# Performance work log

Measured on AMD Instinct MI355X. Metric: run time of the kernel, lower is better.

## Reference

```python
import jax, jax.numpy as jnp
import numpy as np

B, T_TEXT, HID = 16, 512, 512
MAX_LEN = 2048
DP_CH, DP_K = 256, 3
PP_CH, PP_K, PP_LAYERS = 384, 5, 5
N_BINS = 256


def conv1d_same(x, w, b, pad):
    # x: [B, C_in, T], w: [C_out, C_in, K] -> [B, C_out, T]
    xp = jnp.pad(x, ((0, 0), (0, 0), (pad, pad)))
    y = jax.lax.conv_general_dilated(xp, w, (1,), 'VALID',
                                     dimension_numbers=('NCH', 'OIH', 'NCH'))
    return y + b[None, :, None]


def channel_ln(x, g, beta, eps=1e-5):
    # LayerNorm over channel dim of [B, C, T] (torch LayerNorm with dim=1)
    m = jnp.mean(x, axis=1, keepdims=True)
    v = jnp.mean((x - m) ** 2, axis=1, keepdims=True)
    return (x - m) / jnp.sqrt(v + eps) * g[None, :, None] + beta[None, :, None]


def sinusoidal_pos(T, dim):
    # fairseq-style sinusoidal embedding, positions start at padding_idx+1 = 1
    half = dim // 2
    inv = jnp.exp(jnp.arange(half, dtype=jnp.float32) * (-np.log(10000.0) / (half - 1)))
    pos = jnp.arange(1, T + 1, dtype=jnp.float32)
    ang = pos[:, None] * inv[None, :]
    return jnp.concatenate([jnp.sin(ang), jnp.cos(ang)], axis=1)  # [T, dim]


def setup_inputs() -> dict:
    key = jax.random.key(0)
    ks = jax.random.split(key, 16)
    sd = lambda fan: 1.0 / np.sqrt(fan)
    inp = {}
    inp['x'] = jax.random.normal(ks[0], (B, T_TEXT, HID), dtype=jnp.float32)
    inp['duration'] = jax.random.randint(ks[1], (B, T_TEXT), 0, 7, dtype=jnp.int32)
    inp['src_mask'] = jnp.zeros((B, T_TEXT), dtype=bool)
    inp['max_len'] = MAX_LEN
    # duration predictor params (2 conv layers + linear)
    inp['dp_w0'] = jax.random.normal(ks[2], (DP_CH, HID, DP_K)) * sd(HID * DP_K)
    inp['dp_w1'] = jax.random.normal(ks[3], (DP_CH, DP_CH, DP_K)) * sd(DP_CH * DP_K)
    inp['dp_b'] = jnp.zeros((2, DP_CH))
    inp['dp_g'] = jnp.ones((2, DP_CH))
    inp['dp_beta'] = jnp.zeros((2, DP_CH))
    inp['dp_lin_w'] = jax.random.normal(ks[4], (DP_CH, 1)) * sd(DP_CH)
    inp['dp_lin_b'] = jnp.zeros((1,))
    # pitch predictor params (5 conv layers + linear, odim=2 for use_uv)
    inp['pp_w0'] = jax.random.normal(ks[5], (PP_CH, HID, PP_K)) * sd(HID * PP_K)
    inp['pp_w_rest'] = jax.random.normal(ks[6], (PP_LAYERS - 1, PP_CH, PP_CH, PP_K)) * sd(PP_CH * PP_K)
    inp['pp_b'] = jnp.zeros((PP_LAYERS, PP_CH))
    inp['pp_g'] = jnp.ones((PP_LAYERS, PP_CH))
    inp['pp_beta'] = jnp.zeros((PP_LAYERS, PP_CH))
    inp['pp_lin_w'] = jax.random.normal(ks[7], (PP_CH, 2)) * sd(PP_CH)
    inp['pp_lin_b'] = jnp.zeros((2,))
    inp['pos_alpha'] = jnp.ones((1,))
    inp['pitch_emb'] = jax.random.normal(ks[8], (N_BINS, HID)) * 0.02
    inp['pitch_bins'] = jnp.linspace(-1.0, 1.0, N_BINS - 1)  # linear quantization, stats min/max
    return inp


def reference(x, duration, src_mask, max_len, dp_w0, dp_w1, dp_b, dp_g, dp_beta,
              dp_lin_w, dp_lin_b, pp_w0, pp_w_rest, pp_b, pp_g, pp_beta,
              pp_lin_w, pp_lin_b, pos_alpha, pitch_emb, pitch_bins):
    Bn, T, H = x.shape
    keep = 1.0 - src_mask.astype(x.dtype)  # [B,T], 1 where valid

    # ---- DurationPredictor (log-domain durations) ----
    h = jnp.transpose(x, (0, 2, 1))  # [B,H,T]
    for i, w in enumerate([dp_w0, dp_w1]):
        h = conv1d_same(h, w, dp_b[i], (DP_K - 1) // 2)
        h = jax.nn.relu(h)
        h = channel_ln(h, dp_g[i], dp_beta[i])
        h = h * keep[:, None, :]
    log_dur = (jnp.einsum('bct,co->bto', h, dp_lin_w) + dp_lin_b) * keep[:, :, None]
    log_dur = log_dur[..., 0]  # [B,T]

    # ---- LengthRegulator: vectorized variable-repeat via searchsorted ----
    cum = jnp.cumsum(duration, axis=1)  # [B,T]
    frames = jnp.arange(max_len)
    tok = jax.vmap(lambda c: jnp.searchsorted(c, frames, side='right'))(cum)  # [B,max_len]
    mel_len = cum[:, -1]
    fmask = (frames[None, :] < mel_len[:, None]).astype(x.dtype)  # [B,max_len]
    mel = jnp.take_along_axis(x, jnp.minimum(tok, T - 1)[..., None], axis=1) * fmask[..., None]

    # ---- VariancePredictor (pitch, odim=2 for f0 + uv) ----
    pe = sinusoidal_pos(max_len, H)  # [max_len, H]
    p = mel + pos_alpha[0] * pe[None]
    p = jnp.transpose(p, (0, 2, 1))  # [B,H,max_len]
    for i in range(PP_LAYERS):
        w = pp_w0 if i == 0 else pp_w_rest[i - 1]
        p = conv1d_same(p, w, pp_b[i], (PP_K - 1) // 2)
        p = jax.nn.relu(p)
        p = channel_ln(p, pp_g[i], pp_beta[i])
    pitch_pred = jnp.einsum('bct,co->bto', p, pp_lin_w) + pp_lin_b  # [B,max_len,2]

    # ---- bucketize f0 channel + embedding add ----
    idx = jnp.searchsorted(pitch_bins, pitch_pred[..., 0], side='left')  # torch.bucketize
    p_embed = pitch_emb[idx]  # [B,max_len,H]
    out = mel + p_embed
    return out, log_dur, pitch_pred, mel_len
```

## Files before the change

kernel.cpp:

```cpp
#include <hip/hip_runtime.h>
#include <cstdint>
#include <cstddef>

constexpr int BB      = 16;
constexpr int T_TEXT  = 512;
constexpr int HID     = 512;
constexpr int MAX_LEN = 2048;
constexpr int DP_CH   = 256;
constexpr int PP_CH   = 384;

typedef unsigned short u16;
typedef unsigned int   u32;
typedef short bf16x8 __attribute__((ext_vector_type(8)));
typedef float f32x4  __attribute__((ext_vector_type(4)));

__device__ __forceinline__ void gload_lds16(const void* g, void* l) {
  __builtin_amdgcn_global_load_lds(
      (const __attribute__((address_space(1))) u32*)g,
      (__attribute__((address_space(3))) u32*)l, 16, 0, 0);
}

__device__ __forceinline__ u16 f2bf(float v) {
  union { float f; u32 u; } a;
  a.f = v;
  u32 r = (a.u + 0x7FFFu + ((a.u >> 16) & 1u)) >> 16;
  return (u16)r;
}
__device__ __forceinline__ float bf2f(u16 h) {
  union { u32 u; float f; } a;
  a.u = (u32)h << 16;
  return a.f;
}

__global__ __launch_bounds__(256) void pack_w_k(const float* __restrict__ w,
                                                u16* __restrict__ p,
                                                int O, int I, int KT) {
  int NF  = O >> 4, NCB = I >> 5;
  int total = KT * NCB * NF * 64;
  int idx = blockIdx.x * 256 + threadIdx.x;
  if (idx >= total) return;
  int l  = idx & 63;
  int f  = (idx >> 6) % NF;
  int cb = ((idx >> 6) / NF) % NCB;
  int k  = (idx >> 6) / (NF * NCB);
  int o  = f * 16 + (l & 15);
  int ib = cb * 32 + (l >> 4) * 8;
  u16* pd = p + ((size_t)((k * NCB + cb) * NF + f)) * 512 + (size_t)l * 8;
#pragma unroll
  for (int j = 0; j < 8; ++j)
    pd[j] = f2bf(w[((size_t)o * I + ib + j) * KT + k]);
}

template <int CIN, int COUT, int KT, int MT, int WM, int WN, int OPAD,
          bool F32OUT, bool ROTATE>
__global__ __launch_bounds__(WM * WN * 64)
void gemm_conv_ln(const u16* __restrict__ a, const u16* __restrict__ wp,
                  const float* __restrict__ bias, const float* __restrict__ gamma,
                  const float* __restrict__ beta,
                  u16* __restrict__ o, float* __restrict__ fo, int T) {
  constexpr int WAVES   = WM * WN;
  constexpr int THREADS = WAVES * 64;
  constexpr int RS    = MT + KT - 1;
  constexpr int NCB   = CIN / 32;
  constexpr int NF    = COUT / 16;
  constexpr int Mfr   = MT / (16 * WM);
  constexpr int Nfr   = NF / WN;
  constexpr int A_ONE = RS * 64;
  constexpr int B_ONE = NF * 1024;
  constexpr int B_OFF = 2 * A_ONE;
  constexpr int NBUFB = ROTATE ? KT : 2;
  constexpr int RED_OFF = B_OFF + NBUFB * B_ONE;
  static_assert(MT % (16 * WM) == 0 && NF % WN == 0, "tiling");
  static_assert((4 * RS) % WAVES == 0, "A chunks split evenly per wave");
  static_assert((NF * 64) % THREADS == 0, "B chunks split evenly");
  constexpr int CPW = 4 * RS / WAVES;

  const int TpIn  = T + KT - 1;
  const int TpOut = T + 2 * OPAD;

  const int tid  = threadIdx.x;
  const int wave = tid >> 6;
  const int lane = tid & 63;
  const int sl   = lane & 15;
  const int q    = lane >> 4;
  const int wm   = wave / WN;
  const int wn   = wave % WN;
  const int waveM0 = wm * Mfr * 16;
  const int f0   = wn * Nfr;
  const int t0   = blockIdx.x * MT;
  const int b    = blockIdx.y;

  extern __shared__ __align__(16) char smem[];

  const u16* abase_g = a + ((size_t)b * TpIn + t0) * CIN;

  auto stageA = [&](int buf, int cb) {
    char* lbase = smem + buf * A_ONE;
#pragma unroll
    for (int j = 0; j < CPW; j += 64) {
      int c   = wave * CPW + j + lane;
      int qc  = c / RS;
      int row = c - qc * RS;
      if (j + lane < CPW)
        gload_lds16(abase_g + (size_t)row * CIN + cb * 32 + qc * 8,
                    lbase + (size_t)(wave * CPW + j) * 16);
    }
  };
  auto stageB = [&](int buf, int k, int cb) {
    const u16* src = wp + ((size_t)(k * NCB + cb) * NF) * 512;
    char* lbase = smem + B_OFF + buf * B_ONE;
#pragma unroll
    for (int i = tid; i < NF * 64; i += THREADS) {
      gload_lds16(src + (size_t)i * 8, lbase + (size_t)(i - lane) * 16);
    }
  };

  f32x4 acc[Mfr][Nfr];
#pragma unroll
  for (int mf = 0; mf < Mfr; ++mf)
#pragma unroll
    for (int nf = 0; nf < Nfr; ++nf) acc[mf][nf] = (f32x4)0.f;

  if constexpr (ROTATE) {
    stageA(0, 0);
#pragma unroll
    for (int j = 0; j < KT; ++j) stageB(j, j, 0);
    asm volatile("s_waitcnt vmcnt(0)" ::: "memory");
    __syncthreads();

    const int r0 = wave % KT;
    for (int cb = 0; cb < NCB; ++cb) {
      if (cb + 1 < NCB) stageA((cb + 1) & 1, cb + 1);
      const char* ab_l = smem + (cb & 1) * A_ONE;
#pragma unroll
      for (int t = 0; t < KT; ++t) {
        int k = r0 + t;
        if (k >= KT) k -= KT;
        const char* bb_l = smem + B_OFF + k * B_ONE;
        bf16x8 A[Mfr], Bf[Nfr];
#pragma unroll
        for (int mf = 0; mf < Mfr; ++mf) {
          int row = waveM0 + mf * 16 + sl + k;
          A[mf] = *(const bf16x8*)(ab_l + (q * RS + row) * 16);
        }
#pragma unroll
        for (int nf = 0; nf < Nfr; ++nf)
          Bf[nf] = *(const bf16x8*)(bb_l + (size_t)(f0 + nf) * 1024 + lane * 16);
        __builtin_amdgcn_s_setprio(1);
#pragma unroll
        for (int nf = 0; nf < Nfr; ++nf)
#pragma unroll
          for (int mf = 0; mf < Mfr; ++mf)
            acc[mf][nf] = __builtin_amdgcn_mfma_f32_16x16x32_bf16(
                A[mf], Bf[nf], acc[mf][nf], 0, 0, 0);
        __builtin_amdgcn_s_setprio(0);
      }
      __syncthreads();
      if (cb + 1 < NCB) {
#pragma unroll
        for (int j = 0; j < KT; ++j) stageB(j, j, cb + 1);
        asm volatile("s_waitcnt vmcnt(0)" ::: "memory");
        __syncthreads();
      }
    }
  } else {
    stageA(0, 0);
    stageB(0, 0, 0);
    asm volatile("s_waitcnt vmcnt(0)" ::: "memory");
    __syncthreads();
    int ab = 0, bb = 0;
    for (int cb = 0; cb < NCB; ++cb) {
      for (int k = 0; k < KT; ++k) {
        if (k + 1 < KT) {
          stageB(bb ^ 1, k + 1, cb);
        } else if (cb + 1 < NCB) {
          stageB(bb ^ 1, 0, cb + 1);
          stageA(ab ^ 1, cb + 1);
        }
        bf16x8 A[Mfr], Bf[Nfr];
        const char* ab_l = smem + ab * A_ONE;
#pragma unroll
        for (int mf = 0; mf < Mfr; ++mf) {
          int row = waveM0 + mf * 16 + sl + k;
          A[mf] = *(const bf16x8*)(ab_l + (q * RS + row) * 16);
        }
        const char* bb_l = smem + B_OFF + bb * B_ONE;
#pragma unroll
        for (int nf = 0; nf < Nfr; ++nf)
          Bf[nf] = *(const bf16x8*)(bb_l + (size_t)(f0 + nf) * 1024 + lane * 16);
#pragma unroll
        for (int nf = 0; nf < Nfr; ++nf)
#pragma unroll
          for (int mf = 0; mf < Mfr; ++mf)
            acc[mf][nf] = __builtin_amdgcn_mfma_f32_16x16x32_bf16(
                A[mf], Bf[nf], acc[mf][nf], 0, 0, 0);
        asm volatile("s_waitcnt vmcnt(0)" ::: "memory");
        __syncthreads();
        bb ^= 1;
        if (k == KT - 1) ab ^= 1;
      }
    }
  }

  float bc[Nfr], gc[Nfr], btc[Nfr];
#pragma unroll
  for (int nf = 0; nf < Nfr; ++nf) {
    int col = (f0 + nf) * 16 + sl;
    bc[nf]  = bias[col];
    gc[nf]  = gamma[col];
    btc[nf] = beta[col];
  }

  float* reds  = (float*)(smem + RED_OFF);
  float* redss = reds + MT * WN;

#pragma unroll
  for (int mf = 0; mf < Mfr; ++mf) {
#pragma unroll
    for (int r = 0; r < 4; ++r) {
      float s = 0.f, ss2 = 0.f;
#pragma unroll
      for (int nf = 0; nf < Nfr; ++nf) {
        float x = acc[mf][nf][r] + bc[nf];
        x = fmaxf(x, 0.f);
        acc[mf][nf][r] = x;
        s += x;
        ss2 = fmaf(x, x, ss2);
      }
#pragma unroll
      for (int off = 1; off < 16; off <<= 1) {
        s   += __shfl_xor(s, off, 64);
        ss2 += __shfl_xor(ss2, off, 64);
      }
      if (sl == 0) {
        int rowb = waveM0 + mf * 16 + q * 4 + r;
        reds[rowb * WN + wn]  = s;
        redss[rowb * WN + wn] = ss2;
      }
    }
  }
  __syncthreads();

#pragma unroll
  for (int mf = 0; mf < Mfr; ++mf) {
#pragma unroll
    for (int r = 0; r < 4; ++r) {
      int rowb = waveM0 + mf * 16 + q * 4 + r;
      float s = 0.f, ss2 = 0.f;
#pragma unroll
      for (int w2 = 0; w2 < WN; ++w2) {
        s   += reds[rowb * WN + w2];
        ss2 += redss[rowb * WN + w2];
      }
      float mean = s * (1.f / COUT);
      float var  = ss2 * (1.f / COUT) - mean * mean;
      float rstd = 1.f / sqrtf(var + 1e-5f);
      int trow = t0 + rowb;
#pragma unroll
      for (int nf = 0; nf < Nfr; ++nf) {
        int col = (f0 + nf) * 16 + sl;
        float y = (acc[mf][nf][r] - mean) * rstd * gc[nf] + btc[nf];
        if constexpr (F32OUT) {
          fo[((size_t)b * T + trow) * COUT + col] = y;
        } else {
          o[((size_t)b * TpOut + OPAD + trow) * COUT + col] = f2bf(y);
        }
      }
    }
  }

  if constexpr (!F32OUT && OPAD > 0) {
    if (blockIdx.x == 0) {
      for (int i = tid; i < OPAD * COUT; i += THREADS) {
        o[(size_t)b * TpOut * COUT + i] = 0;
        o[((size_t)b * TpOut + OPAD + T) * COUT + i] = 0;
      }
    }
  }
}

constexpr int gemm_lds(int MT, int KT, int COUT, int WN_, int nbufb) {
  return 2 * (MT + KT - 1) * 64 + nbufb * (COUT / 16) * 1024 + MT * WN_ * 8;
}

__global__ __launch_bounds__(256) void split_x_k(const float* __restrict__ x,
                                                 u16* __restrict__ xb) {
  int b = blockIdx.y;
  int row = blockIdx.x * 4 + (threadIdx.x >> 6);
  int lane = threadIdx.x & 63;
  if (row >= T_TEXT + 2) return;
  size_t out = ((size_t)b * (T_TEXT + 2) + row) * HID;
  if (row == 0 || row == T_TEXT + 1) {
    for (int h = lane; h < HID; h += 64) xb[out + h] = 0;
    return;
  }
  const float* xr = x + ((size_t)b * T_TEXT + row - 1) * HID;
  for (int h = lane; h < HID; h += 64) xb[out + h] = f2bf(xr[h]);
}

__global__ __launch_bounds__(256) void dp_head_k(const float* __restrict__ h,
                                                 const float* __restrict__ w,
                                                 const float* __restrict__ b,
                                                 float* __restrict__ out) {
  int tid = threadIdx.x;
  int wv = tid >> 6, lane = tid & 63;
  int row = blockIdx.x * 4 + wv;
  const float* hr = h + (size_t)row * DP_CH;
  float s = 0.f;
  for (int c = lane; c < DP_CH; c += 64) s = fmaf(hr[c], w[c], s);
#pragma unroll
  for (int off = 1; off < 64; off <<= 1) s += __shfl_xor(s, off, 64);
  if (lane == 0) out[row] = s + b[0];
}

__global__ __launch_bounds__(512) void cumsum_k(const int* __restrict__ dur,
                                                int* __restrict__ cum,
                                                float* __restrict__ mel_len_out) {
  __shared__ int s[T_TEXT];
  int b = blockIdx.x, t = threadIdx.x;
  s[t] = dur[b * T_TEXT + t];
  __syncthreads();
  for (int off = 1; off < T_TEXT; off <<= 1) {
    int add = (t >= off) ? s[t - off] : 0;
    __syncthreads();
    s[t] += add;
    __syncthreads();
  }
  cum[b * T_TEXT + t] = s[t];
  if (t == T_TEXT - 1) mel_len_out[b] = (float)s[t];
}

__global__ __launch_bounds__(256) void build_p_k(const float* __restrict__ x,
                                                 const int* __restrict__ cum,
                                                 const float* __restrict__ alpha_p,
                                                 u16* __restrict__ pb) {
  __shared__ int cs[T_TEXT];
  int b = blockIdx.y, tid = threadIdx.x;
  for (int i = tid; i < T_TEXT; i += 256) cs[i] = cum[b * T_TEXT + i];
  __syncthreads();
  int row = blockIdx.x * 4 + (tid >> 6);
  int lane = tid & 63;
  if (row >= MAX_LEN + 4) return;
  size_t out = ((size_t)b * (MAX_LEN + 4) + row) * HID;
  if (row < 2 || row >= MAX_LEN + 2) {
    for (int h = lane; h < HID; h += 64) pb[out + h] = 0;
    return;
  }
  int f = row - 2;
  int lo = 0, hi = T_TEXT;
  while (lo < hi) {
    int mid = (lo + hi) >> 1;
    if (cs[mid] <= f) lo = mid + 1; else hi = mid;
  }
  int src = min(lo, T_TEXT - 1);
  float fm = (f < cs[T_TEXT - 1]) ? 1.f : 0.f;
  float alpha = alpha_p[0];
  const float* xr = x + ((size_t)b * T_TEXT + src) * HID;
  float posf = (float)(f + 1);
  const float kfac = -0.03611898185f;
  for (int h = lane; h < HID / 2; h += 64) {
    float inv = expf((float)h * kfac);
    float ang = posf * inv;
    float sv, cv;
    sincosf(ang, &sv, &cv);
    pb[out + h]           = f2bf(fmaf(alpha, sv, xr[h] * fm));
    pb[out + h + HID / 2] = f2bf(fmaf(alpha, cv, xr[h + HID / 2] * fm));
  }
}

__global__ __launch_bounds__(256) void final_head_k(
    const u16* __restrict__ p, const float* __restrict__ x,
    const int* __restrict__ cum, const float* __restrict__ lw,
    const float* __restrict__ lb, const float* __restrict__ bins,
    const float* __restrict__ emb, float* __restrict__ out0,
    float* __restrict__ pred) {
  __shared__ int cs[T_TEXT];
  int b = blockIdx.y, tid = threadIdx.x;
  for (int i = tid; i < T_TEXT; i += 256) cs[i] = cum[b * T_TEXT + i];
  __syncthreads();
  int wv = tid >> 6, lane = tid & 63;
  int f = blockIdx.x * 4 + wv;
  size_t row = (size_t)b * MAX_LEN + f;
  const u16* prr = p + row * PP_CH;
  float s0 = 0.f, s1 = 0.f;
  for (int c = lane; c < PP_CH; c += 64) {
    float v = bf2f(prr[c]);
    s0 = fmaf(v, lw[2 * c], s0);
    s1 = fmaf(v, lw[2 * c + 1], s1);
  }
#pragma unroll
  for (int off = 1; off < 64; off <<= 1) {
    s0 += __shfl_xor(s0, off, 64);
    s1 += __shfl_xor(s1, off, 64);
  }
  float p0 = s0 + lb[0];
  float p1 = s1 + lb[1];
  if (lane == 0) {
    pred[row * 2] = p0;
    pred[row * 2 + 1] = p1;
  }
  int lo = 0, hi = 255;
  while (lo < hi) {
    int mid = (lo + hi) >> 1;
    if (bins[mid] < p0) lo = mid + 1; else hi = mid;
  }
  int lo2 = 0, hi2 = T_TEXT;
  while (lo2 < hi2) {
    int mid = (lo2 + hi2) >> 1;
    if (cs[mid] <= f) lo2 = mid + 1; else hi2 = mid;
  }
  int src = min(lo2, T_TEXT - 1);
  float fm = (f < cs[T_TEXT - 1]) ? 1.f : 0.f;
  const float* xr = x + ((size_t)b * T_TEXT + src) * HID;
  const float* er = emb + (size_t)lo * HID;
  float* orow = out0 + row * HID;
  for (int h = lane; h < HID; h += 64) orow[h] = fmaf(xr[h], fm, er[h]);
}

extern "C" void kernel_launch(void* const* d_in, const int* in_sizes, int n_in,
                              void* d_out, int out_size, void* d_ws,
                              size_t ws_size, hipStream_t stream) {
  (void)in_sizes; (void)n_in; (void)out_size; (void)ws_size;

  const float* x          = (const float*)d_in[0];
  const int*   duration   = (const int*)d_in[1];
  const float* dp_w0      = (const float*)d_in[4];
  const float* dp_w1      = (const float*)d_in[5];
  const float* dp_b       = (const float*)d_in[6];
  const float* dp_g       = (const float*)d_in[7];
  const float* dp_beta    = (const float*)d_in[8];
  const float* dp_lin_w   = (const float*)d_in[9];
  const float* dp_lin_b   = (const float*)d_in[10];
  const float* pp_w0      = (const float*)d_in[11];
  const float* pp_w_rest  = (const float*)d_in[12];
  const float* pp_b       = (const float*)d_in[13];
  const float* pp_g       = (const float*)d_in[14];
  const float* pp_beta    = (const float*)d_in[15];
  const float* pp_lin_w   = (const float*)d_in[16];
  const float* pp_lin_b   = (const float*)d_in[17];
  const float* pos_alpha  = (const float*)d_in[18];
  const float* pitch_emb  = (const float*)d_in[19];
  const float* pitch_bins = (const float*)d_in[20];

  char* w8 = (char*)d_ws;
  size_t off = 0;
  auto alloc = [&](size_t bytes) {
    char* pp = w8 + off;
    off += (bytes + 255) & ~(size_t)255;
    return pp;
  };
  u16*   xb    = (u16*)alloc((size_t)BB * 514 * 512 * 2);
  u16*   dp1   = (u16*)alloc((size_t)BB * 514 * 256 * 2);
  float* dp2   = (float*)alloc((size_t)BB * 512 * 256 * 4);
  u16*   Pb    = (u16*)alloc((size_t)BB * 2052 * 512 * 2);
  u16*   ppA   = (u16*)alloc((size_t)BB * 2052 * 384 * 2);
  u16*   ppB   = (u16*)alloc((size_t)BB * 2052 * 384 * 2);
  u16*   pfin  = (u16*)alloc((size_t)BB * 2048 * 384 * 2);
  u16*   pwdp0 = (u16*)alloc((size_t)3 * 512 * 256 * 2);
  u16*   pwdp1 = (u16*)alloc((size_t)3 * 256 * 256 * 2);
  u16*   pwpp0 = (u16*)alloc((size_t)5 * 512 * 384 * 2);
  u16*   pwppr = (u16*)alloc((size_t)4 * 5 * 384 * 384 * 2);
  int*   cum   = (int*)alloc((size_t)BB * T_TEXT * 4);

  float* out0       = (float*)d_out;
  float* log_dur    = out0 + (size_t)BB * MAX_LEN * HID;
  float* pitch_pred = log_dur + (size_t)BB * T_TEXT;
  float* mel_len    = pitch_pred + (size_t)BB * MAX_LEN * 2;

  auto pk = [&](const float* src, u16* dst, int O, int I, int KT) {
    int tot = KT * (I / 32) * (O / 16) * 64;
    pack_w_k<<<dim3((tot + 255) / 256), dim3(256), 0, stream>>>(src, dst, O, I, KT);
  };
  pk(dp_w0, pwdp0, 256, 512, 3);
  pk(dp_w1, pwdp1, 256, 256, 3);
  pk(pp_w0, pwpp0, 384, 512, 5);
  for (int l = 0; l < 4; ++l)
    pk(pp_w_rest + (size_t)l * 384 * 384 * 5,
       pwppr + (size_t)l * (5 * 384 * 384), 384, 384, 5);

  split_x_k<<<dim3(129, BB), dim3(256), 0, stream>>>(x, xb);
  cumsum_k<<<dim3(BB), dim3(512), 0, stream>>>(duration, cum, mel_len);

  constexpr int LDS_DP = gemm_lds(64, 3, 256, 2, 2);
  gemm_conv_ln<512, 256, 3, 64, 2, 2, 1, false, false>
      <<<dim3(8, BB), dim3(256), LDS_DP, stream>>>(
          xb, pwdp0, dp_b, dp_g, dp_beta, dp1, nullptr, T_TEXT);
  gemm_conv_ln<256, 256, 3, 64, 2, 2, 1, true, false>
      <<<dim3(8, BB), dim3(256), LDS_DP, stream>>>(
          dp1, pwdp1, dp_b + 256, dp_g + 256, dp_beta + 256,
          nullptr, dp2, T_TEXT);
  dp_head_k<<<dim3(BB * T_TEXT / 4), dim3(256), 0, stream>>>(dp2, dp_lin_w,
                                                             dp_lin_b, log_dur);

  build_p_k<<<dim3(513, BB), dim3(256), 0, stream>>>(x, cum, pos_alpha, Pb);

  constexpr int LDS_PP = gemm_lds(128, 5, 384, 4, 5);
  gemm_conv_ln<512, 384, 5, 128, 2, 4, 2, false, true>
      <<<dim3(16, BB), dim3(512), LDS_PP, stream>>>(
          Pb, pwpp0, pp_b, pp_g, pp_beta, ppA, nullptr, MAX_LEN);
  gemm_conv_ln<384, 384, 5, 128, 2, 4, 2, false, true>
      <<<dim3(16, BB), dim3(512), LDS_PP, stream>>>(
          ppA, pwppr + 0 * (5 * 384 * 384),
          pp_b + 384, pp_g + 384, pp_beta + 384, ppB, nullptr, MAX_LEN);
  gemm_conv_ln<384, 384, 5, 128, 2, 4, 2, false, true>
      <<<dim3(16, BB), dim3(512), LDS_PP, stream>>>(
          ppB, pwppr + 1 * (5 * 384 * 384),
          pp_b + 768, pp_g + 768, pp_beta + 768, ppA, nullptr, MAX_LEN);
  gemm_conv_ln<384, 384, 5, 128, 2, 4, 2, false, true>
      <<<dim3(16, BB), dim3(512), LDS_PP, stream>>>(
          ppA, pwppr + 2 * (5 * 384 * 384),
          pp_b + 1152, pp_g + 1152, pp_beta + 1152, ppB, nullptr, MAX_LEN);
  gemm_conv_ln<384, 384, 5, 128, 2, 4, 0, false, true>
      <<<dim3(16, BB), dim3(512), LDS_PP, stream>>>(
          ppB, pwppr + 3 * (5 * 384 * 384),
          pp_b + 1536, pp_g + 1536, pp_beta + 1536, pfin, nullptr, MAX_LEN);

  final_head_k<<<dim3(MAX_LEN / 4, BB), dim3(256), 0, stream>>>(
      pfin, x, cum, pp_lin_w, pp_lin_b, pitch_bins, pitch_emb, out0, pitch_pred);
}
```

Before: 443.1 us.

## Software-pipeline weight staging per tap and precompute positional embedding table

The pitch-predictor conv GEMM now issues B-tile loads two steps ahead, one tap per step, using partial vmcnt waits and a single barrier per step. This replaces the old scheme, which loaded all taps, drained fully and used two syncthreads per channel block, so memory stalls were exposed. Separately, the sinusoidal positional table is computed once by a new kernel rather than per batch inside build_p_k. This removes redundant exp and sincos work but adds an extra global read. The hardcoded vmcnt values depend on how many loads each thread issues, which is fragile if the tile configuration changes.

```diff
diff --git a/kernel.cpp b/kernel.cpp
--- a/kernel.cpp
+++ b/kernel.cpp
@@ -18,6 +18,13 @@
   __builtin_amdgcn_global_load_lds(
       (const __attribute__((address_space(1))) u32*)g,
       (__attribute__((address_space(3))) u32*)l, 16, 0, 0);
+}
+
+template <int N> __device__ __forceinline__ void vm_wait() {
+  if constexpr (N == 0)      asm volatile("s_waitcnt vmcnt(0)" ::: "memory");
+  else if constexpr (N == 3) asm volatile("s_waitcnt vmcnt(3)" ::: "memory");
+  else if constexpr (N == 5) asm volatile("s_waitcnt vmcnt(5)" ::: "memory");
+  else static_assert(N == 0, "unsupported vmcnt literal");
 }
 
 __device__ __forceinline__ u16 f2bf(float v) {
@@ -52,7 +59,7 @@
 }
 
 template <int CIN, int COUT, int KT, int MT, int WM, int WN, int OPAD,
-          bool F32OUT, bool ROTATE>
+          bool F32OUT, bool PIPE>
 __global__ __launch_bounds__(WM * WN * 64)
 void gemm_conv_ln(const u16* __restrict__ a, const u16* __restrict__ wp,
                   const float* __restrict__ bias, const float* __restrict__ gamma,
@@ -68,8 +75,9 @@
   constexpr int A_ONE = RS * 64;
   constexpr int B_ONE = NF * 1024;
   constexpr int B_OFF = 2 * A_ONE;
-  constexpr int NBUFB = ROTATE ? KT : 2;
+  constexpr int NBUFB = PIPE ? KT : 2;
   constexpr int RED_OFF = B_OFF + NBUFB * B_ONE;
+  constexpr int NSTEPS = NCB * KT;
   static_assert(MT % (16 * WM) == 0 && NF % WN == 0, "tiling");
   static_assert((4 * RS) % WAVES == 0, "A chunks split evenly per wave");
   static_assert((NF * 64) % THREADS == 0, "B chunks split evenly");
@@ -121,31 +129,38 @@
 #pragma unroll
     for (int nf = 0; nf < Nfr; ++nf) acc[mf][nf] = (f32x4)0.f;
 
-  if constexpr (ROTATE) {
+  if constexpr (PIPE) {
     stageA(0, 0);
-#pragma unroll
-    for (int j = 0; j < KT; ++j) stageB(j, j, 0);
-    asm volatile("s_waitcnt vmcnt(0)" ::: "memory");
-    __syncthreads();
-
-    const int r0 = wave % KT;
+    stageB(0, 0, 0);
+    stageB(1 % KT, 1 % KT, 0);
+    vm_wait<3>();
+    __builtin_amdgcn_s_barrier();
+
     for (int cb = 0; cb < NCB; ++cb) {
-      if (cb + 1 < NCB) stageA((cb + 1) & 1, cb + 1);
       const char* ab_l = smem + (cb & 1) * A_ONE;
 #pragma unroll
-      for (int t = 0; t < KT; ++t) {
-        int k = r0 + t;
-        if (k >= KT) k -= KT;
-        const char* bb_l = smem + B_OFF + k * B_ONE;
+      for (int j = 0; j < KT; ++j) {
+        const int s = cb * KT + j;
+        __builtin_amdgcn_sched_barrier(0);
+
         bf16x8 A[Mfr], Bf[Nfr];
+        const char* bb_l = smem + B_OFF + j * B_ONE;
 #pragma unroll
         for (int mf = 0; mf < Mfr; ++mf) {
-          int row = waveM0 + mf * 16 + sl + k;
+          int row = waveM0 + mf * 16 + sl + j;
           A[mf] = *(const bf16x8*)(ab_l + (q * RS + row) * 16);
         }
 #pragma unroll
         for (int nf = 0; nf < Nfr; ++nf)
           Bf[nf] = *(const bf16x8*)(bb_l + (size_t)(f0 + nf) * 1024 + lane * 16);
+
+        const bool boundary = (j == 0 && cb + 1 < NCB);
+        if (boundary) stageA((cb + 1) & 1, cb + 1);
+        if (s + 2 < NSTEPS) {
+          const int s2 = s + 2;
+          stageB(s2 % KT, s2 % KT, s2 / KT);
+        }
+
         __builtin_amdgcn_s_setprio(1);
 #pragma unroll
         for (int nf = 0; nf < Nfr; ++nf)
@@ -154,13 +169,15 @@
             acc[mf][nf] = __builtin_amdgcn_mfma_f32_16x16x32_bf16(
                 A[mf], Bf[nf], acc[mf][nf], 0, 0, 0);
         __builtin_amdgcn_s_setprio(0);
-      }
-      __syncthreads();
-      if (cb + 1 < NCB) {
-#pragma unroll
-        for (int j = 0; j < KT; ++j) stageB(j, j, cb + 1);
-        asm volatile("s_waitcnt vmcnt(0)" ::: "memory");
-        __syncthreads();
+
+        __builtin_amdgcn_sched_barrier(0);
+        if (s + 2 < NSTEPS) {
+          if (boundary) vm_wait<5>();
+          else          vm_wait<3>();
+        } else {
+          vm_wait<0>();
+        }
+        __builtin_amdgcn_s_barrier();
       }
     }
   } else {
@@ -330,9 +347,26 @@
   if (t == T_TEXT - 1) mel_len_out[b] = (float)s[t];
 }
 
+__global__ __launch_bounds__(256) void pe_k(float* __restrict__ pe) {
+  int f = blockIdx.x * 4 + (threadIdx.x >> 6);
+  int lane = threadIdx.x & 63;
+  float posf = (float)(f + 1);
+  const float kfac = -0.03611898185f;
+  float* pr = pe + (size_t)f * HID;
+  for (int h = lane; h < HID / 2; h += 64) {
+    float inv = expf((float)h * kfac);
+    float ang = posf * inv;
+    float sv, cv;
+    sincosf(ang, &sv, &cv);
+    pr[h]           = sv;
+    pr[h + HID / 2] = cv;
+  }
+}
+
 __global__ __launch_bounds__(256) void build_p_k(const float* __restrict__ x,
                                                  const int* __restrict__ cum,
                                                  const float* __restrict__ alpha_p,
+                                                 const float* __restrict__ pe,
                                                  u16* __restrict__ pb) {
   __shared__ int cs[T_TEXT];
   int b = blockIdx.y, tid = threadIdx.x;
@@ -356,16 +390,9 @@
   float fm = (f < cs[T_TEXT - 1]) ? 1.f : 0.f;
   float alpha = alpha_p[0];
   const float* xr = x + ((size_t)b * T_TEXT + src) * HID;
-  float posf = (float)(f + 1);
-  const float kfac = -0.03611898185f;
-  for (int h = lane; h < HID / 2; h += 64) {
-    float inv = expf((float)h * kfac);
-    float ang = posf * inv;
-    float sv, cv;
-    sincosf(ang, &sv, &cv);
-    pb[out + h]           = f2bf(fmaf(alpha, sv, xr[h] * fm));
-    pb[out + h + HID / 2] = f2bf(fmaf(alpha, cv, xr[h + HID / 2] * fm));
-  }
+  const float* pr = pe + (size_t)f * HID;
+  for (int h = lane; h < HID; h += 64)
+    pb[out + h] = f2bf(fmaf(alpha, pr[h], xr[h] * fm));
 }
 
 __global__ __launch_bounds__(256) void final_head_k(
@@ -456,6 +483,7 @@
   u16*   ppA   = (u16*)alloc((size_t)BB * 2052 * 384 * 2);
   u16*   ppB   = (u16*)alloc((size_t)BB * 2052 * 384 * 2);
   u16*   pfin  = (u16*)alloc((size_t)BB * 2048 * 384 * 2);
+  float* peT   = (float*)alloc((size_t)MAX_LEN * HID * 4);
   u16*   pwdp0 = (u16*)alloc((size_t)3 * 512 * 256 * 2);
   u16*   pwdp1 = (u16*)alloc((size_t)3 * 256 * 256 * 2);
   u16*   pwpp0 = (u16*)alloc((size_t)5 * 512 * 384 * 2);
@@ -480,6 +508,7 @@
 
   split_x_k<<<dim3(129, BB), dim3(256), 0, stream>>>(x, xb);
   cumsum_k<<<dim3(BB), dim3(512), 0, stream>>>(duration, cum, mel_len);
+  pe_k<<<dim3(MAX_LEN / 4), dim3(256), 0, stream>>>(peT);
 
   constexpr int LDS_DP = gemm_lds(64, 3, 256, 2, 2);
   gemm_conv_ln<512, 256, 3, 64, 2, 2, 1, false, false>
@@ -492,7 +521,7 @@
   dp_head_k<<<dim3(BB * T_TEXT / 4), dim3(256), 0, stream>>>(dp2, dp_lin_w,
                                                              dp_lin_b, log_dur);
 
-  build_p_k<<<dim3(513, BB), dim3(256), 0, stream>>>(x, cum, pos_alpha, Pb);
+  build_p_k<<<dim3(513, BB), dim3(256), 0, stream>>>(x, cum, pos_alpha, peT, Pb);
 
   constexpr int LDS_PP = gemm_lds(128, 5, 384, 4, 5);
   gemm_conv_ln<512, 384, 5, 128, 2, 4, 2, false, true>
```

After: 412.1 us (median of 2 runs). 1.08x faster.
